# Optimization experiments

Measured on AMD Instinct MI355X. Metric: run time of the kernel, lower is better.

Reference implementation:

```python
import jax, jax.numpy as jnp
import numpy as np

SCALE = 1.0 / np.sqrt(128.0).astype(np.float32)  # 1/sqrt(head_dim)


def setup_inputs() -> dict:
    key = jax.random.key(0)
    kq, kk, kv = jax.random.split(key, 3)
    B, S, D = 32, 2048, 128
    q = jax.random.normal(kq, (B, S, D), dtype=jnp.float32)
    k = jax.random.normal(kk, (B, S, D), dtype=jnp.float32)
    v = jax.random.normal(kv, (B, S, D), dtype=jnp.float32)
    return {"q": q, "k": k, "v": v}


def reference(q, k, v):
    # attention = bmm(q, k^T) * scale ; softmax over last (key) dim; bmm with v
    scores = jnp.einsum("bsd,btd->bst", q, k) * SCALE  # [B, S, S]
    attn = jax.nn.softmax(scores, axis=-1)
    return jnp.einsum("bst,btd->bsd", attn, v)  # [B, S, D]
```

## Files before the change

### kernel.cpp

```cpp
#include <hip/hip_runtime.h>
#include <math.h>
#include <stdint.h>

typedef __bf16 bf16_t;
typedef __bf16 bf16x2 __attribute__((ext_vector_type(2)));
typedef __bf16 bf16x4 __attribute__((ext_vector_type(4)));
typedef __bf16 bf16x8 __attribute__((ext_vector_type(8)));
typedef float f32x4 __attribute__((ext_vector_type(4)));
typedef float f32x16 __attribute__((ext_vector_type(16)));

#define NB   32
#define SEQ  2048
#define HD   128
#define SCALE 0.08838834764831845f
#define LOG2E 1.4426950408889634f

__device__ __forceinline__ float fast_exp2(float x) {
#if __has_builtin(__builtin_amdgcn_exp2f)
  return __builtin_amdgcn_exp2f(x);
#else
  return exp2f(x);
#endif
}

__global__ __launch_bounds__(256) void prep_kernel(
    const float* __restrict__ Q, const float* __restrict__ K,
    const float* __restrict__ V, bf16_t* __restrict__ Qs,
    bf16_t* __restrict__ Kb, bf16_t* __restrict__ Vt)
{
  const int b = blockIdx.x;
  const int tid = threadIdx.x;
  if (b < 4096) {
    const bool isQ = (b < 2048);
    const float* src = isQ ? Q : K;
    bf16_t* dst = isQ ? Qs : Kb;
    const float sc = isQ ? (SCALE * LOG2E) : 1.0f;
    size_t base4 = (size_t)(isQ ? b : b - 2048) * 1024;
#pragma unroll
    for (int i = 0; i < 4; ++i) {
      size_t idx = base4 + tid + i * 256;
      float4 x = ((const float4*)src)[idx];
      bf16x4 y;
      y[0] = (bf16_t)(x.x * sc); y[1] = (bf16_t)(x.y * sc);
      y[2] = (bf16_t)(x.z * sc); y[3] = (bf16_t)(x.w * sc);
      ((bf16x4*)dst)[idx] = y;
    }
  } else {
    __shared__ float tile[64][65];
    const int bt = b - 4096;
    const int batch = bt >> 6;
    const int rem = bt & 63;
    const int s0 = (rem >> 1) * 64;
    const int d0 = (rem & 1) * 64;
#pragma unroll
    for (int i = 0; i < 4; ++i) {
      int e = tid + i * 256;
      int s = e >> 4, dq = e & 15;
      float4 x = *(const float4*)&V[((size_t)batch * SEQ + s0 + s) * HD + d0 + dq * 4];
      tile[s][dq * 4 + 0] = x.x;
      tile[s][dq * 4 + 1] = x.y;
      tile[s][dq * 4 + 2] = x.z;
      tile[s][dq * 4 + 3] = x.w;
    }
    __syncthreads();
#pragma unroll
    for (int i = 0; i < 2; ++i) {
      int g = tid + i * 256;
      int d = g >> 3, sg = g & 7;
      bf16x8 w;
#pragma unroll
      for (int j = 0; j < 8; ++j) w[j] = (bf16_t)tile[sg * 8 + j][d];
      *(bf16x8*)&Vt[((size_t)batch * HD + d0 + d) * SEQ + s0 + sg * 8] = w;
    }
  }
}

__global__ __launch_bounds__(256) void fa12_kernel(
    const bf16_t* __restrict__ Qs, const bf16_t* __restrict__ Kbf,
    const bf16_t* __restrict__ Vt, float* __restrict__ O)
{
  __shared__ __attribute__((aligned(16))) bf16_t Ksw[2][64 * 128];
  __shared__ __attribute__((aligned(16))) bf16_t Vsw[2][128 * 64];
  __shared__ float mlbuf[2][2][32];

  const int tid  = threadIdx.x;
  const int lane = tid & 63;
  const int wq   = tid >> 6;
  const int hi   = lane >> 5;
  const int q31  = lane & 31;
  const int pair = wq >> 1;
  const int sub  = wq & 1;
  const int koff = sub * 32;

  const int batch = blockIdx.x >> 5;
  const int qt    = blockIdx.x & 31;

  const bf16_t* Qb = Qs + ((size_t)batch * SEQ + qt * 64 + pair * 32) * HD;
  const bf16_t* Kb = Kbf + (size_t)batch * SEQ * HD;
  const bf16_t* Vb = Vt + (size_t)batch * HD * SEQ;
  float*        Ob = O + ((size_t)batch * SEQ + qt * 64) * HD;

  bf16x8 bq[8];
#pragma unroll
  for (int dc = 0; dc < 8; ++dc)
    bq[dc] = *(const bf16x8*)&Qb[(size_t)q31 * HD + dc * 16 + hi * 8];

  f32x16 o[4];
#pragma unroll
  for (int dt = 0; dt < 4; ++dt)
#pragma unroll
    for (int r = 0; r < 16; ++r) o[dt][r] = 0.f;
  float m_r = -INFINITY, l_r = 0.0f;

  auto stage = [&](int buf, int kb) {
#pragma unroll
    for (int i = 0; i < 4; ++i) {
      int row = wq * 16 + i * 4 + (lane >> 4);
      int gk = (lane & 15) ^ (row & 15);
      const bf16_t* gp = Kb + (size_t)(kb + row) * HD + gk * 8;
      __builtin_amdgcn_global_load_lds(
          (const __attribute__((address_space(1))) void*)gp,
          (__attribute__((address_space(3))) void*)&Ksw[buf][(wq * 16 + i * 4) * 128],
          16, 0, 0);
    }
#pragma unroll
    for (int i = 0; i < 4; ++i) {
      int d = wq * 32 + i * 8 + (lane >> 3);
      int gv = (lane & 7) ^ (d & 7);
      const bf16_t* gp = Vb + (size_t)d * SEQ + kb + gv * 8;
      __builtin_amdgcn_global_load_lds(
          (const __attribute__((address_space(1))) void*)gp,
          (__attribute__((address_space(3))) void*)&Vsw[buf][(wq * 32 + i * 8) * 64],
          16, 0, 0);
    }
  };

  stage(0, 0);

  for (int t = 0; t < SEQ / 64; ++t) {
    __syncthreads();
    if (t + 1 < SEQ / 64) stage((t + 1) & 1, (t + 1) * 64);

    const bf16_t* Ks = &Ksw[t & 1][0];
    const bf16_t* Vs = &Vsw[t & 1][0];

    f32x16 s;
#pragma unroll
    for (int r = 0; r < 16; ++r) s[r] = 0.f;
    {
      const int row = koff + q31;
      const int rsw = row & 15;
#pragma unroll
      for (int dc = 0; dc < 8; ++dc) {
        bf16x8 ak = *(const bf16x8*)&Ks[row * 128 + (((dc * 2 + hi) ^ rsw) * 8)];
        s = __builtin_amdgcn_mfma_f32_32x32x16_bf16(ak, bq[dc], s, 0, 0, 0);
      }
    }

    float mx = s[0];
#pragma unroll
    for (int r = 1; r < 16; ++r) mx = fmaxf(mx, s[r]);
    mx = fmaxf(mx, __shfl_xor(mx, 32));

    if (!__all(mx <= m_r + 8.0f)) {
      const float mnew = fmaxf(m_r, mx);
      const float alpha = fast_exp2(m_r - mnew);
      m_r = mnew;
      l_r *= alpha;
#pragma unroll
      for (int dt = 0; dt < 4; ++dt) o[dt] = o[dt] * alpha;
    }

    float ls = 0.f;
#pragma unroll
    for (int r = 0; r < 16; ++r) {
      float p = fast_exp2(s[r] - m_r);
      s[r] = p; ls += p;
    }
    ls += __shfl_xor(ls, 32);
    l_r += ls;

    uint32_t pk[8];
#pragma unroll
    for (int i = 0; i < 8; ++i) {
      union { bf16x2 v; uint32_t u; } c;
      c.v[0] = (bf16_t)s[2 * i];
      c.v[1] = (bf16_t)s[2 * i + 1];
      pk[i] = c.u;
    }
    uint32_t t0 = __shfl_xor((int)(hi ? pk[0] : pk[2]), 32);
    uint32_t t1 = __shfl_xor((int)(hi ? pk[1] : pk[3]), 32);
    uint32_t t2 = __shfl_xor((int)(hi ? pk[4] : pk[6]), 32);
    uint32_t t3 = __shfl_xor((int)(hi ? pk[5] : pk[7]), 32);
    bf16x8 bp0, bp1;
    {
      union { bf16x8 v; uint32_t w[4]; } B;
      if (hi) { B.w[0] = t0; B.w[1] = t1; B.w[2] = pk[2]; B.w[3] = pk[3]; }
      else    { B.w[0] = pk[0]; B.w[1] = pk[1]; B.w[2] = t0; B.w[3] = t1; }
      bp0 = B.v;
      if (hi) { B.w[0] = t2; B.w[1] = t3; B.w[2] = pk[6]; B.w[3] = pk[7]; }
      else    { B.w[0] = pk[4]; B.w[1] = pk[5]; B.w[2] = t2; B.w[3] = t3; }
      bp1 = B.v;
    }

    {
      const int g0 = (koff >> 3) + hi;
      const int g1 = g0 + 2;
#pragma unroll
      for (int dt = 0; dt < 4; ++dt) {
        const int d = dt * 32 + q31;
        const int dsw = d & 7;
        bf16x8 av0 = *(const bf16x8*)&Vs[d * 64 + ((g0 ^ dsw) * 8)];
        o[dt] = __builtin_amdgcn_mfma_f32_32x32x16_bf16(av0, bp0, o[dt], 0, 0, 0);
        bf16x8 av1 = *(const bf16x8*)&Vs[d * 64 + ((g1 ^ dsw) * 8)];
        o[dt] = __builtin_amdgcn_mfma_f32_32x32x16_bf16(av1, bp1, o[dt], 0, 0, 0);
      }
    }
  }

  __syncthreads();
  float* obuf = (pair == 0) ? (float*)&Ksw[0][0] : (float*)&Vsw[0][0];

  if (sub == 1) {
    if (hi == 0) {
      mlbuf[pair][0][q31] = m_r;
      mlbuf[pair][1][q31] = l_r;
    }
#pragma unroll
    for (int dt = 0; dt < 4; ++dt)
#pragma unroll
      for (int r = 0; r < 16; ++r) {
        int d = dt * 32 + (r & 3) + 8 * (r >> 2) + 4 * hi;
        obuf[q31 * 132 + d] = o[dt][r];
      }
  }
  __syncthreads();
  if (sub == 0) {
    float m1 = mlbuf[pair][0][q31];
    float l1 = mlbuf[pair][1][q31];
    float m = fmaxf(m_r, m1);
    float e0 = fast_exp2(m_r - m);
    float e1 = fast_exp2(m1 - m);
    float inv = 1.0f / (l_r * e0 + l1 * e1);
    float f0 = e0 * inv, f1 = e1 * inv;
#pragma unroll
    for (int dt = 0; dt < 4; ++dt)
#pragma unroll
      for (int r = 0; r < 16; ++r) {
        int d = dt * 32 + (r & 3) + 8 * (r >> 2) + 4 * hi;
        obuf[q31 * 132 + d] = o[dt][r] * f0 + obuf[q31 * 132 + d] * f1;
      }
  }
  __syncthreads();
  {
    const int tid2 = sub * 64 + lane;
#pragma unroll
    for (int i = 0; i < 8; ++i) {
      int idx = tid2 + i * 128;
      int q = idx >> 5;
      int dg = idx & 31;
      float4 v = *(const float4*)&obuf[q * 132 + dg * 4];
      *(float4*)&Ob[(size_t)(pair * 32 + q) * HD + dg * 4] = v;
    }
  }
}

#define BM   64
#define BN   64
#define KPAD 8
#define VPAD 8
#define PPAD 8

__global__ __launch_bounds__(256) void fa_fallback(
    const float* __restrict__ Q, const float* __restrict__ K,
    const float* __restrict__ V, float* __restrict__ O)
{
  __shared__ __attribute__((aligned(16))) bf16_t Ksh[BN][HD + KPAD];
  __shared__ __attribute__((aligned(16))) bf16_t Vsh[HD][BN + VPAD];
  __shared__ __attribute__((aligned(16))) bf16_t Psh[4][16][BN + PPAD];

  const int tid = threadIdx.x;
  const int lane = tid & 63;
  const int wq = tid >> 6;
  const int quad = lane >> 4;
  const int l15 = lane & 15;
  const int bid = blockIdx.x;
  const int batch = bid >> 5;
  const int qt = bid & 31;

  const float* Qb = Q + (size_t)batch * SEQ * HD + (size_t)qt * BM * HD;
  const float* Kb = K + (size_t)batch * SEQ * HD;
  const float* Vb = V + (size_t)batch * SEQ * HD;
  float* Ob = O + (size_t)batch * SEQ * HD + (size_t)qt * BM * HD;

  bf16x8 aq[4];
  {
    const int qrow = wq * 16 + l15;
#pragma unroll
    for (int kf = 0; kf < 4; ++kf) {
      const float* qp = Qb + (size_t)qrow * HD + kf * 32 + quad * 8;
      float4 x0 = *(const float4*)(qp);
      float4 x1 = *(const float4*)(qp + 4);
      bf16x8 a;
      a[0] = (bf16_t)(x0.x * SCALE); a[1] = (bf16_t)(x0.y * SCALE);
      a[2] = (bf16_t)(x0.z * SCALE); a[3] = (bf16_t)(x0.w * SCALE);
      a[4] = (bf16_t)(x1.x * SCALE); a[5] = (bf16_t)(x1.y * SCALE);
      a[6] = (bf16_t)(x1.z * SCALE); a[7] = (bf16_t)(x1.w * SCALE);
      aq[kf] = a;
    }
  }

  f32x4 o[8];
#pragma unroll
  for (int t = 0; t < 8; ++t) { o[t][0]=0.f; o[t][1]=0.f; o[t][2]=0.f; o[t][3]=0.f; }
  float m_r = -INFINITY, l_r = 0.0f;
  const int vkp = (tid & 31) * 2;
  const int vg = tid >> 5;
  float4 kreg[8], vreg[8];

#pragma unroll
  for (int i = 0; i < 8; ++i) {
    int v = tid + i * 256, row = v >> 5, c4 = (v & 31) * 4;
    kreg[i] = *(const float4*)(Kb + (size_t)row * HD + c4);
  }
#pragma unroll
  for (int i = 0; i < 4; ++i) {
    int d0 = (vg + i * 8) * 4;
    const float* vp0 = Vb + (size_t)vkp * HD + d0;
    vreg[2 * i] = *(const float4*)vp0;
    vreg[2 * i + 1] = *(const float4*)(vp0 + HD);
  }

  for (int kb = 0; kb < SEQ; kb += BN) {
    __syncthreads();
#pragma unroll
    for (int i = 0; i < 8; ++i) {
      int v = tid + i * 256, row = v >> 5, c4 = (v & 31) * 4;
      float4 kv = kreg[i];
      bf16x4 kk;
      kk[0]=(bf16_t)kv.x; kk[1]=(bf16_t)kv.y; kk[2]=(bf16_t)kv.z; kk[3]=(bf16_t)kv.w;
      *(bf16x4*)&Ksh[row][c4] = kk;
    }
#pragma unroll
    for (int i = 0; i < 4; ++i) {
      int d0 = (vg + i * 8) * 4;
      float4 a0 = vreg[2 * i], a1 = vreg[2 * i + 1];
      bf16x2 p0; p0[0]=(bf16_t)a0.x; p0[1]=(bf16_t)a1.x;
      bf16x2 p1; p1[0]=(bf16_t)a0.y; p1[1]=(bf16_t)a1.y;
      bf16x2 p2; p2[0]=(bf16_t)a0.z; p2[1]=(bf16_t)a1.z;
      bf16x2 p3; p3[0]=(bf16_t)a0.w; p3[1]=(bf16_t)a1.w;
      *(bf16x2*)&Vsh[d0 + 0][vkp] = p0;
      *(bf16x2*)&Vsh[d0 + 1][vkp] = p1;
      *(bf16x2*)&Vsh[d0 + 2][vkp] = p2;
      *(bf16x2*)&Vsh[d0 + 3][vkp] = p3;
    }
    __syncthreads();

    const int kbn = kb + BN;
    if (kbn < SEQ) {
#pragma unroll
      for (int i = 0; i < 8; ++i) {
        int v = tid + i * 256, row = v >> 5, c4 = (v & 31) * 4;
        kreg[i] = *(const float4*)(Kb + (size_t)(kbn + row) * HD + c4);
      }
#pragma unroll
      for (int i = 0; i < 4; ++i) {
        int d0 = (vg + i * 8) * 4;
        const float* vp0 = Vb + (size_t)(kbn + vkp) * HD + d0;
        vreg[2 * i] = *(const float4*)vp0;
        vreg[2 * i + 1] = *(const float4*)(vp0 + HD);
      }
    }

    f32x4 s[4];
#pragma unroll
    for (int ct = 0; ct < 4; ++ct) { s[ct][0]=0.f; s[ct][1]=0.f; s[ct][2]=0.f; s[ct][3]=0.f; }
#pragma unroll
    for (int kf = 0; kf < 4; ++kf)
#pragma unroll
      for (int ct = 0; ct < 4; ++ct) {
        bf16x8 ak = *(const bf16x8*)&Ksh[ct * 16 + l15][kf * 32 + quad * 8];
        s[ct] = __builtin_amdgcn_mfma_f32_16x16x32_bf16(ak, aq[kf], s[ct], 0, 0, 0);
      }

    float mx = s[0][0];
#pragma unroll
    for (int ct = 0; ct < 4; ++ct)
#pragma unroll
      for (int r = 0; r < 4; ++r) mx = fmaxf(mx, s[ct][r]);
    mx = fmaxf(mx, __shfl_xor(mx, 16));
    mx = fmaxf(mx, __shfl_xor(mx, 32));
    float mnew = fmaxf(m_r, mx);
    float alpha = __expf(m_r - mnew);
    m_r = mnew;
    float ls = 0.f;
#pragma unroll
    for (int ct = 0; ct < 4; ++ct)
#pragma unroll
      for (int r = 0; r < 4; ++r) {
        float p = __expf(s[ct][r] - mnew);
        s[ct][r] = p; ls += p;
      }
    ls += __shfl_xor(ls, 16);
    ls += __shfl_xor(ls, 32);
    l_r = l_r * alpha + ls;

#pragma unroll
    for (int ct = 0; ct < 4; ++ct) {
      bf16x4 pp;
      pp[0]=(bf16_t)s[ct][0]; pp[1]=(bf16_t)s[ct][1];
      pp[2]=(bf16_t)s[ct][2]; pp[3]=(bf16_t)s[ct][3];
      *(bf16x4*)&Psh[wq][l15][ct * 16 + quad * 4] = pp;
    }
    asm volatile("s_waitcnt lgkmcnt(0)" ::: "memory");
    bf16x8 ap0 = *(const bf16x8*)&Psh[wq][l15][quad * 8];
    bf16x8 ap1 = *(const bf16x8*)&Psh[wq][l15][32 + quad * 8];

#pragma unroll
    for (int t = 0; t < 8; ++t) {
      o[t][0]*=alpha; o[t][1]*=alpha; o[t][2]*=alpha; o[t][3]*=alpha;
    }
#pragma unroll
    for (int t = 0; t < 8; ++t) {
      bf16x8 av0 = *(const bf16x8*)&Vsh[t * 16 + l15][quad * 8];
      o[t] = __builtin_amdgcn_mfma_f32_16x16x32_bf16(av0, ap0, o[t], 0, 0, 0);
      bf16x8 av1 = *(const bf16x8*)&Vsh[t * 16 + l15][32 + quad * 8];
      o[t] = __builtin_amdgcn_mfma_f32_16x16x32_bf16(av1, ap1, o[t], 0, 0, 0);
    }
  }

  float inv = 1.0f / l_r;
  const int qrow = wq * 16 + l15;
#pragma unroll
  for (int t = 0; t < 8; ++t) {
    float4 w;
    w.x = o[t][0]*inv; w.y = o[t][1]*inv; w.z = o[t][2]*inv; w.w = o[t][3]*inv;
    *(float4*)&Ob[(size_t)qrow * HD + t * 16 + quad * 4] = w;
  }
}

extern "C" void kernel_launch(void* const* d_in, const int* in_sizes, int n_in,
                              void* d_out, int out_size, void* d_ws, size_t ws_size,
                              hipStream_t stream) {
  const float* q = (const float*)d_in[0];
  const float* k = (const float*)d_in[1];
  const float* v = (const float*)d_in[2];
  float* out = (float*)d_out;

  const size_t elems = (size_t)NB * SEQ * HD;
  const size_t need = elems * 2 * 3;

  if (ws_size >= need) {
    bf16_t* Qs = (bf16_t*)d_ws;
    bf16_t* Kb = Qs + elems;
    bf16_t* Vt = Kb + elems;
    prep_kernel<<<6144, 256, 0, stream>>>(q, k, v, Qs, Kb, Vt);
    fa12_kernel<<<NB * (SEQ / 64), 256, 0, stream>>>(Qs, Kb, Vt, out);
  } else {
    fa_fallback<<<NB * (SEQ / BM), 256, 0, stream>>>(q, k, v, out);
  }
}
```

Before: 238.5 us.

## Double query tile to 128 rows per block with 512 threads sharing K/V tiles

Each block now covers 128 query rows with 8 waves (four pairs) instead of 64 rows with 4 waves. Every K/V tile staged in LDS is therefore shared by twice as many queries, which halves global K/V traffic per query and the per-thread staging work. The epilogue merge buffer and the m/l scratch are repacked into a single larger shared array to hold four pairs. The cost is more LDS per block (about 67 KB) and half as many blocks, which may reduce occupancy and leave the grid with fewer blocks to balance across CUs.

```diff
diff --git a/kernel.cpp b/kernel.cpp
--- a/kernel.cpp
+++ b/kernel.cpp
@@ -75,13 +75,13 @@
   }
 }
 
-__global__ __launch_bounds__(256) void fa12_kernel(
+__global__ __launch_bounds__(512, 4) void fa13_kernel(
     const bf16_t* __restrict__ Qs, const bf16_t* __restrict__ Kbf,
     const bf16_t* __restrict__ Vt, float* __restrict__ O)
 {
-  __shared__ __attribute__((aligned(16))) bf16_t Ksw[2][64 * 128];
-  __shared__ __attribute__((aligned(16))) bf16_t Vsw[2][128 * 64];
-  __shared__ float mlbuf[2][2][32];
+  __shared__ __attribute__((aligned(16))) char smem[68608];
+  bf16_t* const Ksw = (bf16_t*)smem;
+  bf16_t* const Vsw = (bf16_t*)(smem + 32768);
 
   const int tid  = threadIdx.x;
   const int lane = tid & 63;
@@ -92,13 +92,13 @@
   const int sub  = wq & 1;
   const int koff = sub * 32;
 
-  const int batch = blockIdx.x >> 5;
-  const int qt    = blockIdx.x & 31;
-
-  const bf16_t* Qb = Qs + ((size_t)batch * SEQ + qt * 64 + pair * 32) * HD;
+  const int batch = blockIdx.x >> 4;
+  const int qt    = blockIdx.x & 15;
+
+  const bf16_t* Qb = Qs + ((size_t)batch * SEQ + qt * 128 + pair * 32) * HD;
   const bf16_t* Kb = Kbf + (size_t)batch * SEQ * HD;
   const bf16_t* Vb = Vt + (size_t)batch * HD * SEQ;
-  float*        Ob = O + ((size_t)batch * SEQ + qt * 64) * HD;
+  float*        Ob = O + ((size_t)batch * SEQ + qt * 128) * HD;
 
   bf16x8 bq[8];
 #pragma unroll
@@ -114,23 +114,23 @@
 
   auto stage = [&](int buf, int kb) {
 #pragma unroll
-    for (int i = 0; i < 4; ++i) {
-      int row = wq * 16 + i * 4 + (lane >> 4);
+    for (int i = 0; i < 2; ++i) {
+      int row = wq * 8 + i * 4 + (lane >> 4);
       int gk = (lane & 15) ^ (row & 15);
       const bf16_t* gp = Kb + (size_t)(kb + row) * HD + gk * 8;
       __builtin_amdgcn_global_load_lds(
           (const __attribute__((address_space(1))) void*)gp,
-          (__attribute__((address_space(3))) void*)&Ksw[buf][(wq * 16 + i * 4) * 128],
+          (__attribute__((address_space(3))) void*)&Ksw[buf * 8192 + (wq * 8 + i * 4) * 128],
           16, 0, 0);
     }
 #pragma unroll
-    for (int i = 0; i < 4; ++i) {
-      int d = wq * 32 + i * 8 + (lane >> 3);
+    for (int i = 0; i < 2; ++i) {
+      int d = wq * 16 + i * 8 + (lane >> 3);
       int gv = (lane & 7) ^ (d & 7);
       const bf16_t* gp = Vb + (size_t)d * SEQ + kb + gv * 8;
       __builtin_amdgcn_global_load_lds(
           (const __attribute__((address_space(1))) void*)gp,
-          (__attribute__((address_space(3))) void*)&Vsw[buf][(wq * 32 + i * 8) * 64],
+          (__attribute__((address_space(3))) void*)&Vsw[buf * 8192 + (wq * 16 + i * 8) * 64],
           16, 0, 0);
     }
   };
@@ -141,8 +141,8 @@
     __syncthreads();
     if (t + 1 < SEQ / 64) stage((t + 1) & 1, (t + 1) * 64);
 
-    const bf16_t* Ks = &Ksw[t & 1][0];
-    const bf16_t* Vs = &Vsw[t & 1][0];
+    const bf16_t* Ks = &Ksw[(t & 1) * 8192];
+    const bf16_t* Vs = &Vsw[(t & 1) * 8192];
 
     f32x16 s;
 #pragma unroll
@@ -219,25 +219,26 @@
   }
 
   __syncthreads();
-  float* obuf = (pair == 0) ? (float*)&Ksw[0][0] : (float*)&Vsw[0][0];
+  float* const sf  = (float*)smem;
+  float* const mlb = (float*)(smem + 67584);
 
   if (sub == 1) {
     if (hi == 0) {
-      mlbuf[pair][0][q31] = m_r;
-      mlbuf[pair][1][q31] = l_r;
+      mlb[pair * 64 + q31]      = m_r;
+      mlb[pair * 64 + 32 + q31] = l_r;
     }
 #pragma unroll
     for (int dt = 0; dt < 4; ++dt)
 #pragma unroll
       for (int r = 0; r < 16; ++r) {
         int d = dt * 32 + (r & 3) + 8 * (r >> 2) + 4 * hi;
-        obuf[q31 * 132 + d] = o[dt][r];
+        sf[pair * 4224 + q31 * 132 + d] = o[dt][r];
       }
   }
   __syncthreads();
   if (sub == 0) {
-    float m1 = mlbuf[pair][0][q31];
-    float l1 = mlbuf[pair][1][q31];
+    float m1 = mlb[pair * 64 + q31];
+    float l1 = mlb[pair * 64 + 32 + q31];
     float m = fmaxf(m_r, m1);
     float e0 = fast_exp2(m_r - m);
     float e1 = fast_exp2(m1 - m);
@@ -248,19 +249,19 @@
 #pragma unroll
       for (int r = 0; r < 16; ++r) {
         int d = dt * 32 + (r & 3) + 8 * (r >> 2) + 4 * hi;
-        obuf[q31 * 132 + d] = o[dt][r] * f0 + obuf[q31 * 132 + d] * f1;
+        float* p = &sf[pair * 4224 + q31 * 132 + d];
+        *p = o[dt][r] * f0 + *p * f1;
       }
   }
   __syncthreads();
   {
-    const int tid2 = sub * 64 + lane;
 #pragma unroll
     for (int i = 0; i < 8; ++i) {
-      int idx = tid2 + i * 128;
+      int idx = tid + i * 512;
       int q = idx >> 5;
       int dg = idx & 31;
-      float4 v = *(const float4*)&obuf[q * 132 + dg * 4];
-      *(float4*)&Ob[(size_t)(pair * 32 + q) * HD + dg * 4] = v;
+      float4 v = *(const float4*)&sf[(q >> 5) * 4224 + (q & 31) * 132 + dg * 4];
+      *(float4*)&Ob[(size_t)q * HD + dg * 4] = v;
     }
   }
 }
@@ -455,7 +456,7 @@
     bf16_t* Kb = Qs + elems;
     bf16_t* Vt = Kb + elems;
     prep_kernel<<<6144, 256, 0, stream>>>(q, k, v, Qs, Kb, Vt);
-    fa12_kernel<<<NB * (SEQ / 64), 256, 0, stream>>>(Qs, Kb, Vt, out);
+    fa13_kernel<<<NB * (SEQ / 128), 512, 0, stream>>>(Qs, Kb, Vt, out);
   } else {
     fa_fallback<<<NB * (SEQ / BM), 256, 0, stream>>>(q, k, v, out);
   }
```

After: 270.2 us. 13.3% more time.
